# Optimization experiments

Hardware: AMD Instinct MI355X
Metric: run time of the kernel (lower is better)

The kernel has to match this reference:

```python
import jax, jax.numpy as jnp
import numpy as np

EMBED_DIM = 512
NUM_HEADS = 8
K_NEAREST = 5
B = 8192
N_MEM = 50000


def setup_inputs() -> dict:
    key = jax.random.key(0)
    ks = jax.random.split(key, 12)
    E = EMBED_DIM
    s = 1.0 / np.sqrt(E)
    inp = {
        "Q": jax.random.normal(ks[0], (B, E), jnp.float32),
        "mem_keys": jax.random.normal(ks[1], (N_MEM, E), jnp.float32),
        "mem_vals": jax.random.normal(ks[2], (N_MEM, E), jnp.float32),
        # pre-projection linears (linear_q/k/v)
        "Wq": jax.random.uniform(ks[3], (E, E), jnp.float32, -s, s),
        "bq": jnp.zeros((E,), jnp.float32),
        "Wk": jax.random.uniform(ks[4], (E, E), jnp.float32, -s, s),
        "bk": jnp.zeros((E,), jnp.float32),
        "Wv": jax.random.uniform(ks[5], (E, E), jnp.float32, -s, s),
        "bv": jnp.zeros((E,), jnp.float32),
        # nn.MultiheadAttention internal in/out projections
        "W_in_q": jax.random.uniform(ks[6], (E, E), jnp.float32, -s, s),
        "W_in_k": jax.random.uniform(ks[7], (E, E), jnp.float32, -s, s),
        "W_in_v": jax.random.uniform(ks[8], (E, E), jnp.float32, -s, s),
        "b_in": jnp.zeros((3 * E,), jnp.float32),
        "W_out": jax.random.uniform(ks[9], (E, E), jnp.float32, -s, s),
        "b_out": jnp.zeros((E,), jnp.float32),
    }
    return inp


def _find_k_nearest(Q, mem_keys, mem_vals, k):
    # squared Euclidean distance; argmax of negative distance == k nearest
    # dists: [B, N]
    sq = jnp.sum(mem_keys * mem_keys, axis=-1)  # [N]
    scores = 2.0 * (Q @ mem_keys.T) - sq[None, :]  # -||q-m||^2 up to const
    _, idx = jax.lax.top_k(scores, k)  # [B, k]
    K = mem_keys[idx]  # [B, k, E]
    V = mem_vals[idx]  # [B, k, E]
    return K, V


def _mha(Q, K, V, W_in_q, W_in_k, W_in_v, b_in, W_out, b_out):
    # Q: [B,1,E], K/V: [B,k,E]; torch nn.MultiheadAttention, batch_first
    E = Q.shape[-1]
    H = NUM_HEADS
    d = E // H
    q = Q @ W_in_q.T + b_in[:E]
    k = K @ W_in_k.T + b_in[E:2 * E]
    v = V @ W_in_v.T + b_in[2 * E:]
    Bsz = Q.shape[0]
    q = q.reshape(Bsz, -1, H, d).transpose(0, 2, 1, 3)  # [B,H,1,d]
    k = k.reshape(Bsz, -1, H, d).transpose(0, 2, 1, 3)  # [B,H,k,d]
    v = v.reshape(Bsz, -1, H, d).transpose(0, 2, 1, 3)
    scores = jnp.einsum("bhqd,bhkd->bhqk", q, k) / jnp.sqrt(jnp.float32(d))
    attn = jax.nn.softmax(scores, axis=-1)
    out = jnp.einsum("bhqk,bhkd->bhqd", attn, v)
    out = out.transpose(0, 2, 1, 3).reshape(Bsz, -1, E)
    return out @ W_out.T + b_out


def reference(Q, mem_keys, mem_vals, Wq, bq, Wk, bk, Wv, bv,
              W_in_q, W_in_k, W_in_v, b_in, W_out, b_out):
    K, V = _find_k_nearest(Q, mem_keys, mem_vals, K_NEAREST)
    Qs = Q[:, None, :]  # [B,1,E]
    Qp = Qs @ Wq.T + bq
    Kp = K @ Wk.T + bk
    Vp = V @ Wv.T + bv
    return _mha(Qp, Kp, Vp, W_in_q, W_in_k, W_in_v, b_in, W_out, b_out)
```

## Files before the change

### kernel.cpp

```cpp
#include <hip/hip_runtime.h>
#include <hip/hip_bf16.h>
#include <hip/hip_fp16.h>

typedef _Float16 f16;
typedef _Float16 f16x8 __attribute__((ext_vector_type(8)));
typedef float f32x4 __attribute__((ext_vector_type(4)));

constexpr int EE     = 512;
constexpr int NMEM   = 50000;
constexpr int BQ     = 8192;
constexpr int NSEG   = 16;
constexpr int SEGLEN = NMEM / NSEG;
constexpr int KVT    = 32;
constexpr int NT32   = (SEGLEN + KVT - 1) / KVT;
constexpr int NC     = 5;
constexpr int NCAND  = NSEG * NC;
constexpr int NRES   = 10;

typedef const __attribute__((address_space(1))) unsigned char* gas_t;
typedef __attribute__((address_space(3))) unsigned char* las_t;
__device__ static inline void g2l16(const void* g, void* l) {
  __builtin_amdgcn_global_load_lds((gas_t)g, (las_t)l, 16, 0, 0);
}

__device__ static inline float pack_si(float s, int li) {
  return __uint_as_float((__float_as_uint(s) & 0xFFFFF000u) | (unsigned)li);
}

__global__ __launch_bounds__(256) void k_prep_keys(const float* __restrict__ mk,
                                                   f16* __restrict__ kh,
                                                   float* __restrict__ sq32,
                                                   double* __restrict__ sq64) {
  int row  = blockIdx.x * 4 + (threadIdx.x >> 6);
  int lane = threadIdx.x & 63;
  const float4* src = (const float4*)(mk + (size_t)row * EE) + lane * 2;
  float4 a = src[0], b = src[1];
  double s = (double)a.x*a.x + (double)a.y*a.y + (double)a.z*a.z + (double)a.w*a.w
           + (double)b.x*b.x + (double)b.y*b.y + (double)b.z*b.z + (double)b.w*b.w;
  f16x8 h;
  h[0]=(f16)a.x; h[1]=(f16)a.y; h[2]=(f16)a.z; h[3]=(f16)a.w;
  h[4]=(f16)b.x; h[5]=(f16)b.y; h[6]=(f16)b.z; h[7]=(f16)b.w;
  *((f16x8*)(kh + (size_t)row * EE) + lane) = h;
  #pragma unroll
  for (int o = 32; o > 0; o >>= 1) s += __shfl_down(s, o);
  if (lane == 0) { sq64[row] = s; sq32[row] = (float)s; }
}

__global__ __launch_bounds__(256) void k_prep_f16(const float* __restrict__ src,
                                                  f16* __restrict__ dst) {
  int row  = blockIdx.x * 4 + (threadIdx.x >> 6);
  int lane = threadIdx.x & 63;
  const float4* s = (const float4*)(src + (size_t)row * EE) + lane * 2;
  float4 a = s[0], b = s[1];
  f16x8 h;
  h[0]=(f16)a.x; h[1]=(f16)a.y; h[2]=(f16)a.z; h[3]=(f16)a.w;
  h[4]=(f16)b.x; h[5]=(f16)b.y; h[6]=(f16)b.z; h[7]=(f16)b.w;
  *((f16x8*)(dst + (size_t)row * EE) + lane) = h;
}

__global__ __launch_bounds__(256) void k_compose(const float* __restrict__ Wq, const float* __restrict__ Wk,
                                                 const float* __restrict__ Wv, const float* __restrict__ Wiq,
                                                 const float* __restrict__ Wik, const float* __restrict__ Wiv,
                                                 f16* __restrict__ Wc) {
  int m = blockIdx.z;
  const float* A = (m == 0) ? Wiq : ((m == 1) ? Wik : Wiv);
  const float* B = (m == 0) ? Wq  : ((m == 1) ? Wk  : Wv);
  f16* C = Wc + (size_t)m * EE * EE;
  __shared__ float As[64][33];
  __shared__ float Bs[32][65];
  int i0 = blockIdx.x * 64, j0 = blockIdx.y * 64;
  int tx = threadIdx.x & 15, ty = threadIdx.x >> 4;
  float acc[4][4] = {};
  for (int kb = 0; kb < EE; kb += 32) {
    __syncthreads();
    #pragma unroll
    for (int v = 0; v < 8; ++v) {
      int idx = threadIdx.x + v * 256;
      As[idx >> 5][idx & 31] = A[(size_t)(i0 + (idx >> 5)) * EE + kb + (idx & 31)];
    }
    #pragma unroll
    for (int v = 0; v < 8; ++v) {
      int idx = threadIdx.x + v * 256;
      Bs[idx >> 6][idx & 63] = B[(size_t)(kb + (idx >> 6)) * EE + j0 + (idx & 63)];
    }
    __syncthreads();
    for (int t = 0; t < 32; ++t) {
      float av[4], bv[4];
      #pragma unroll
      for (int u = 0; u < 4; ++u) av[u] = As[ty*4+u][t];
      #pragma unroll
      for (int u = 0; u < 4; ++u) bv[u] = Bs[t][tx*4+u];
      #pragma unroll
      for (int a = 0; a < 4; ++a)
        #pragma unroll
        for (int b = 0; b < 4; ++b) acc[a][b] = fmaf(av[a], bv[b], acc[a][b]);
    }
  }
  #pragma unroll
  for (int a = 0; a < 4; ++a)
    #pragma unroll
    for (int b = 0; b < 4; ++b)
      C[(size_t)(i0 + ty*4 + a) * EE + j0 + tx*4 + b] = (f16)acc[a][b];
}

__global__ void k_bias(const float* __restrict__ Wiq, const float* __restrict__ Wik,
                       const float* __restrict__ Wiv, const float* __restrict__ bqv,
                       const float* __restrict__ bkv, const float* __restrict__ bvv,
                       const float* __restrict__ b_in, float* __restrict__ bc) {
  int m = blockIdx.x;
  const float* Wi = (m == 0) ? Wiq : ((m == 1) ? Wik : Wiv);
  const float* bb = (m == 0) ? bqv : ((m == 1) ? bkv : bvv);
  for (int i = threadIdx.x; i < EE; i += blockDim.x) {
    float s = 0.f;
    for (int t = 0; t < EE; ++t) s = fmaf(Wi[(size_t)i * EE + t], bb[t], s);
    bc[m * EE + i] = s + b_in[m * EE + i];
  }
}

__global__ void k_cvtw(const float* __restrict__ W, f16* __restrict__ Wo) {
  int i = blockIdx.x * 256 + threadIdx.x;
  Wo[i] = (f16)W[i];
}

__global__ __launch_bounds__(256, 2) void k_stage1(const f16* __restrict__ Qh,
                                                   const f16* __restrict__ Kh,
                                                   const float* __restrict__ sq32,
                                                   int* __restrict__ part_i,
                                                   float* __restrict__ part_s) {
  const int rb  = blockIdx.x;
  const int seg = blockIdx.y;
  const int tid = threadIdx.x;
  const int w   = tid >> 6;
  const int l   = tid & 63;
  const int lc  = l & 15, lp = l >> 4;
  const int seg_start = seg * SEGLEN;
  const int seg_end   = seg_start + SEGLEN;

  __shared__ f16   Bt[2][KVT * 520];
  __shared__ float sqs[2][KVT];

  const int rowbase = rb * 128 + w * 32;
  f16x8 a0[16], a1[16];
  {
    const f16* base0 = Qh + (size_t)(rowbase + lc) * EE + lp * 8;
    const f16* base1 = base0 + (size_t)16 * EE;
    #pragma unroll
    for (int ks = 0; ks < 16; ++ks) {
      asm volatile("global_load_dwordx4 %0, %1, off"
                   : "=v"(a0[ks]) : "v"(base0 + ks * 32) : "memory");
      asm volatile("global_load_dwordx4 %0, %1, off"
                   : "=v"(a1[ks]) : "v"(base1 + ks * 32) : "memory");
    }
    asm volatile("s_waitcnt vmcnt(0)" ::: "memory");
    __builtin_amdgcn_sched_barrier(0);
  }

  float ts0[NC], ts1[NC];
  #pragma unroll
  for (int i = 0; i < NC; ++i) { ts0[i] = -3.0e38f; ts1[i] = -3.0e38f; }

#define INS1(TS, PV) do { \
    if (__ballot((PV) > TS[NC-1])) { \
      float _nv = ((PV) > TS[NC-1]) ? (PV) : TS[NC-1]; \
      TS[NC-1] = _nv; \
      _Pragma("unroll") \
      for (int _i = NC - 1; _i > 0; --_i) { \
        float _mx = fmaxf(TS[_i], TS[_i-1]); \
        float _mn = fminf(TS[_i], TS[_i-1]); \
        TS[_i-1] = _mx; TS[_i] = _mn; \
      } \
    } \
  } while (0)

  #define STAGE(buf, tt) do { \
      int kk = seg_start + (tt) * KVT; \
      _Pragma("unroll") \
      for (int j = 0; j < 8; ++j) { \
        int key = kk + w * 8 + j; \
        key = key < NMEM ? key : NMEM - 1; \
        g2l16(Kh + (size_t)key * EE + l * 8, &Bt[buf][(w*8 + j) * 520]); \
      } \
      if (tid < KVT) { \
        int kq = kk + tid; \
        float v = 6.0e38f; \
        if (kq < seg_end) v = sq32[kq]; \
        sqs[buf][tid] = v; \
      } \
    } while (0)

  STAGE(0, 0);
  for (int t = 0; t < NT32; ++t) {
    const int c = t & 1;
    __syncthreads();
    if (t + 1 < NT32) STAGE(c ^ 1, t + 1);

    f32x4 A00 = {0,0,0,0}, A01 = {0,0,0,0}, A10 = {0,0,0,0}, A11 = {0,0,0,0};
    #pragma unroll
    for (int ks = 0; ks < 16; ++ks) {
      f16x8 kf0 = *(const f16x8*)&Bt[c][lc * 520 + ks * 32 + lp * 8];
      f16x8 kf1 = *(const f16x8*)&Bt[c][(16 + lc) * 520 + ks * 32 + lp * 8];
      A00 = __builtin_amdgcn_mfma_f32_16x16x32_f16(kf0, a0[ks], A00, 0, 0, 0);
      A01 = __builtin_amdgcn_mfma_f32_16x16x32_f16(kf0, a1[ks], A01, 0, 0, 0);
      A10 = __builtin_amdgcn_mfma_f32_16x16x32_f16(kf1, a0[ks], A10, 0, 0, 0);
      A11 = __builtin_amdgcn_mfma_f32_16x16x32_f16(kf1, a1[ks], A11, 0, 0, 0);
    }
    f32x4 q0 = *(const f32x4*)&sqs[c][lp * 4];
    f32x4 q1 = *(const f32x4*)&sqs[c][16 + lp * 4];
    f32x4 s00 = 2.0f * A00 - q0;
    f32x4 s01 = 2.0f * A01 - q0;
    f32x4 s10 = 2.0f * A10 - q1;
    f32x4 s11 = 2.0f * A11 - q1;
    const int li0 = t * KVT + lp * 4;
    const int li1 = li0 + 16;
    #pragma unroll
    for (int r = 0; r < 4; ++r) {
      INS1(ts0, pack_si(s00[r], li0 + r));
      INS1(ts0, pack_si(s10[r], li1 + r));
      INS1(ts1, pack_si(s01[r], li0 + r));
      INS1(ts1, pack_si(s11[r], li1 + r));
    }
  }
  #undef STAGE

  #pragma unroll
  for (int d = 16; d <= 32; d <<= 1) {
    float os[NC];
    #pragma unroll
    for (int i = 0; i < NC; ++i) os[i] = __shfl_xor(ts0[i], d);
    #pragma unroll
    for (int j = 0; j < NC; ++j) INS1(ts0, os[j]);
    #pragma unroll
    for (int i = 0; i < NC; ++i) os[i] = __shfl_xor(ts1[i], d);
    #pragma unroll
    for (int j = 0; j < NC; ++j) INS1(ts1, os[j]);
  }
#undef INS1
  if (l < 16) {
    int row = rowbase + lc;
    #pragma unroll
    for (int i = 0; i < NC; ++i) {
      unsigned u = __float_as_uint(ts0[i]);
      part_i[(size_t)row * NCAND + seg * NC + i] = seg_start + (int)(u & 0xFFFu);
      part_s[(size_t)row * NCAND + seg * NC + i] = ts0[i];
    }
  } else if (l < 32) {
    int row = rowbase + 16 + lc;
    #pragma unroll
    for (int i = 0; i < NC; ++i) {
      unsigned u = __float_as_uint(ts1[i]);
      part_i[(size_t)row * NCAND + seg * NC + i] = seg_start + (int)(u & 0xFFFu);
      part_s[(size_t)row * NCAND + seg * NC + i] = ts1[i];
    }
  }
}

__global__ __launch_bounds__(64) void k_rescore(const float* __restrict__ Q,
                                                const float* __restrict__ mk,
                                                const double* __restrict__ sq64,
                                                const int* __restrict__ part_i,
                                                const float* __restrict__ part_s,
                                                int* __restrict__ idx5) {
  const int row = blockIdx.x;
  const int l = threadIdx.x;
  const float* Qr = Q + (size_t)row * EE;
  float q[8];
  #pragma unroll
  for (int i = 0; i < 8; ++i) q[i] = Qr[l + 64*i];
  float s0 = part_s[(size_t)row * NCAND + l];
  int   i0 = part_i[(size_t)row * NCAND + l];
  float s1 = (l < NCAND - 64) ? part_s[(size_t)row * NCAND + 64 + l] : -3.0e38f;
  int   i1 = (l < NCAND - 64) ? part_i[(size_t)row * NCAND + 64 + l] : 0;

  double bs[5] = {-1e300, -1e300, -1e300, -1e300, -1e300};
  int    bi[5] = {0, 0, 0, 0, 0};
  #pragma unroll
  for (int p = 0; p < NRES; ++p) {
    bool pick0 = (s0 >= s1);
    float m  = pick0 ? s0 : s1;
    int   mi = pick0 ? i0 : i1;
    int   code = (l << 1) | (pick0 ? 0 : 1);
    #pragma unroll
    for (int o = 32; o > 0; o >>= 1) {
      float mo = __shfl_xor(m, o);
      int   io = __shfl_xor(mi, o);
      int   co = __shfl_xor(code, o);
      if (mo > m || (mo == m && co < code)) { m = mo; mi = io; code = co; }
    }
    if ((code >> 1) == l) { if (code & 1) s1 = -3.0e38f; else s0 = -3.0e38f; }
    const float* kr = mk + (size_t)mi * EE;
    double pd = 0.0;
    #pragma unroll
    for (int i = 0; i < 8; ++i) pd += (double)q[i] * (double)kr[l + 64*i];
    #pragma unroll
    for (int o = 32; o > 0; o >>= 1) pd += __shfl_down(pd, o);
    if (l == 0) {
      double s = 2.0 * pd - sq64[mi];
      if (s > bs[4]) {
        bs[4] = s; bi[4] = mi;
        #pragma unroll
        for (int i = 4; i > 0; --i) {
          if (bs[i] > bs[i-1]) {
            double tf = bs[i]; bs[i] = bs[i-1]; bs[i-1] = tf;
            int    tx = bi[i]; bi[i] = bi[i-1]; bi[i-1] = tx;
          }
        }
      }
    }
  }
  if (l == 0) {
    #pragma unroll
    for (int i = 0; i < 5; ++i) idx5[(size_t)row*5 + i] = bi[i];
  }
}

template <int GATHER, int AF16, int OUTF32>
__global__ __launch_bounds__(256) void k_pgemm128(const int* __restrict__ gidx, const void* __restrict__ Asrc,
                                                  const f16* __restrict__ B, const float* __restrict__ bias,
                                                  void* __restrict__ outp) {
  __shared__ f16 As[128][72];
  __shared__ f16 Bs[64][72];
  const int tid = threadIdx.x;
  const int wv = tid >> 6, l = tid & 63, lc = l & 15, lp = l >> 4;
  const int m0 = blockIdx.x * 128, n0 = blockIdx.y * 64;
  const int r0 = tid >> 3;
  const int cb = (tid & 7) * 8;
  const f16*   arf[4];
  const float* ar32[4];
  #pragma unroll
  for (int v = 0; v < 4; ++v) {
    int row = m0 + r0 + v * 32;
    int gi = GATHER ? gidx[row] : row;
    if (AF16) arf[v]  = (const f16*)Asrc + (size_t)gi * EE;
    else      ar32[v] = (const float*)Asrc + (size_t)gi * EE;
  }
  const f16* br0 = B + (size_t)(n0 + r0) * EE;
  const f16* br1 = B + (size_t)(n0 + r0 + 32) * EE;
  f32x4 acc[2][4] = {{{0,0,0,0},{0,0,0,0},{0,0,0,0},{0,0,0,0}},
                     {{0,0,0,0},{0,0,0,0},{0,0,0,0},{0,0,0,0}}};
  for (int kb = 0; kb < EE; kb += 64) {
    __syncthreads();
    #pragma unroll
    for (int v = 0; v < 4; ++v) {
      if (AF16) {
        *(f16x8*)&As[r0 + v*32][cb] = *(const f16x8*)(arf[v] + kb + cb);
      } else {
        float4 x0 = *(const float4*)(ar32[v] + kb + cb);
        float4 x1 = *(const float4*)(ar32[v] + kb + cb + 4);
        f16x8 h;
        h[0]=(f16)x0.x; h[1]=(f16)x0.y; h[2]=(f16)x0.z; h[3]=(f16)x0.w;
        h[4]=(f16)x1.x; h[5]=(f16)x1.y; h[6]=(f16)x1.z; h[7]=(f16)x1.w;
        *(f16x8*)&As[r0 + v*32][cb] = h;
      }
    }
    *(f16x8*)&Bs[r0][cb]      = *(const f16x8*)(br0 + kb + cb);
    *(f16x8*)&Bs[r0 + 32][cb] = *(const f16x8*)(br1 + kb + cb);
    __syncthreads();
    #pragma unroll
    for (int ks = 0; ks < 2; ++ks) {
      f16x8 a0 = *(const f16x8*)&As[wv*32 + lc][ks*32 + lp*8];
      f16x8 a1 = *(const f16x8*)&As[wv*32 + 16 + lc][ks*32 + lp*8];
      #pragma unroll
      for (int f = 0; f < 4; ++f) {
        f16x8 b = *(const f16x8*)&Bs[f*16 + lc][ks*32 + lp*8];
        acc[0][f] = __builtin_amdgcn_mfma_f32_16x16x32_f16(a0, b, acc[0][f], 0, 0, 0);
        acc[1][f] = __builtin_amdgcn_mfma_f32_16x16x32_f16(a1, b, acc[1][f], 0, 0, 0);
      }
    }
  }
  #pragma unroll
  for (int g = 0; g < 2; ++g) {
    #pragma unroll
    for (int f = 0; f < 4; ++f) {
      int col = n0 + f*16 + lc;
      float bsv = bias[col];
      #pragma unroll
      for (int rr = 0; rr < 4; ++rr) {
        int row = m0 + wv*32 + g*16 + lp*4 + rr;
        float v = acc[g][f][rr] + bsv;
        if (OUTF32) ((float*)outp)[(size_t)row * EE + col] = v;
        else        ((f16*)outp)[(size_t)row * EE + col] = (f16)v;
      }
    }
  }
}

__global__ __launch_bounds__(256) void k_attn(const f16* __restrict__ qp, const f16* __restrict__ kp,
                                              const f16* __restrict__ vp, f16* __restrict__ ao) {
  int row = blockIdx.x * 4 + (threadIdx.x >> 6);
  int l = threadIdx.x & 63;
  int h = l >> 3, sl = l & 7;
  const f16* q = qp + (size_t)row * EE + h * 64 + sl * 8;
  float qv[8];
  #pragma unroll
  for (int i = 0; i < 8; ++i) qv[i] = (float)q[i];
  float sc[5];
  #pragma unroll
  for (int j = 0; j < 5; ++j) {
    const f16* kr = kp + ((size_t)row * 5 + j) * EE + h * 64 + sl * 8;
    float p = 0.f;
    #pragma unroll
    for (int i = 0; i < 8; ++i) p = fmaf(qv[i], (float)kr[i], p);
    p += __shfl_xor(p, 1); p += __shfl_xor(p, 2); p += __shfl_xor(p, 4);
    sc[j] = p * 0.125f;
  }
  float mx = fmaxf(fmaxf(fmaxf(sc[0], sc[1]), fmaxf(sc[2], sc[3])), sc[4]);
  float sum = 0.f;
  #pragma unroll
  for (int j = 0; j < 5; ++j) { sc[j] = __expf(sc[j] - mx); sum += sc[j]; }
  float inv = 1.0f / sum;
  float o[8] = {};
  #pragma unroll
  for (int j = 0; j < 5; ++j) {
    const f16* vr = vp + ((size_t)row * 5 + j) * EE + h * 64 + sl * 8;
    float aw = sc[j] * inv;
    #pragma unroll
    for (int i = 0; i < 8; ++i) o[i] = fmaf(aw, (float)vr[i], o[i]);
  }
  f16* dst = ao + (size_t)row * EE + h * 64 + sl * 8;
  #pragma unroll
  for (int i = 0; i < 8; ++i) dst[i] = (f16)o[i];
}

extern "C" void kernel_launch(void* const* d_in, const int* in_sizes, int n_in,
                              void* d_out, int out_size, void* d_ws, size_t ws_size,
                              hipStream_t stream) {
  const float* Q    = (const float*)d_in[0];
  const float* mk   = (const float*)d_in[1];
  const float* mv   = (const float*)d_in[2];
  const float* Wq   = (const float*)d_in[3];
  const float* bq   = (const float*)d_in[4];
  const float* Wk   = (const float*)d_in[5];
  const float* bk   = (const float*)d_in[6];
  const float* Wv   = (const float*)d_in[7];
  const float* bv   = (const float*)d_in[8];
  const float* Wiq  = (const float*)d_in[9];
  const float* Wik  = (const float*)d_in[10];
  const float* Wiv  = (const float*)d_in[11];
  const float* b_in = (const float*)d_in[12];
  const float* Wo   = (const float*)d_in[13];
  const float* bo   = (const float*)d_in[14];

  char* w = (char*)d_ws;
  size_t off = 0;
  auto alloc = [&](size_t bytes) { size_t o = off; off += (bytes + 255) & ~(size_t)255; return (void*)(w + o); };
  f16*    Kh     = (f16*)   alloc((size_t)NMEM * EE * 2);
  f16*    Qh     = (f16*)   alloc((size_t)BQ * EE * 2);
  float*  sq32   = (float*) alloc((size_t)NMEM * 4);
  double* sq64   = (double*)alloc((size_t)NMEM * 8);
  f16*    Wc     = (f16*)   alloc((size_t)3 * EE * EE * 2);
  f16*    Wo16   = (f16*)   alloc((size_t)EE * EE * 2);
  float*  bc     = (float*) alloc((size_t)3 * EE * 4);
  int*    part_i = (int*)   alloc((size_t)BQ * NCAND * 4);
  float*  part_s = (float*) alloc((size_t)BQ * NCAND * 4);
  int*    idx5   = (int*)   alloc((size_t)BQ * 5 * 4);
  f16*    qp     = (f16*)   alloc((size_t)BQ * EE * 2);
  f16*    vp     = (f16*)   alloc((size_t)BQ * 5 * EE * 2);
  f16*    ao     = Qh;
  size_t need_big = off + (size_t)NMEM * EE * 2 + (size_t)BQ * 5 * EE * 2 + 4096;
  bool big = (ws_size >= need_big);
  f16* Vh = nullptr;
  f16* kp;
  if (big) {
    Vh = (f16*)alloc((size_t)NMEM * EE * 2);
    kp = (f16*)alloc((size_t)BQ * 5 * EE * 2);
  } else {
    kp = Kh;
  }
  (void)in_sizes; (void)n_in; (void)out_size;

  k_prep_keys<<<NMEM / 4, 256, 0, stream>>>(mk, Kh, sq32, sq64);
  k_prep_f16<<<BQ / 4, 256, 0, stream>>>(Q, Qh);
  if (big) k_prep_f16<<<NMEM / 4, 256, 0, stream>>>(mv, Vh);
  k_compose<<<dim3(8, 8, 3), 256, 0, stream>>>(Wq, Wk, Wv, Wiq, Wik, Wiv, Wc);
  k_bias<<<3, 256, 0, stream>>>(Wiq, Wik, Wiv, bq, bk, bv, b_in, bc);
  k_cvtw<<<(EE * EE) / 256, 256, 0, stream>>>(Wo, Wo16);
  k_stage1<<<dim3(BQ / 128, NSEG), 256, 0, stream>>>(Qh, Kh, sq32, part_i, part_s);
  k_rescore<<<BQ, 64, 0, stream>>>(Q, mk, sq64, part_i, part_s, idx5);
  k_pgemm128<0,1,0><<<dim3(BQ / 128, 8), 256, 0, stream>>>(nullptr, Qh, Wc, bc, qp);
  if (big) {
    k_pgemm128<1,1,0><<<dim3(BQ * 5 / 128, 8), 256, 0, stream>>>(idx5, Kh, Wc + (size_t)EE * EE, bc + EE, kp);
    k_pgemm128<1,1,0><<<dim3(BQ * 5 / 128, 8), 256, 0, stream>>>(idx5, Vh, Wc + (size_t)2 * EE * EE, bc + 2 * EE, vp);
  } else {
    k_pgemm128<1,0,0><<<dim3(BQ * 5 / 128, 8), 256, 0, stream>>>(idx5, mk, Wc + (size_t)EE * EE, bc + EE, kp);
    k_pgemm128<1,0,0><<<dim3(BQ * 5 / 128, 8), 256, 0, stream>>>(idx5, mv, Wc + (size_t)2 * EE * EE, bc + 2 * EE, vp);
  }
  k_attn<<<BQ / 4, 256, 0, stream>>>(qp, kp, vp, ao);
  k_pgemm128<0,1,1><<<dim3(BQ / 128, 8), 256, 0, stream>>>(nullptr, ao, Wo16, bo, d_out);
}
```

Baseline: 746.6 us.

## Pre-swizzle keys into MFMA fragment layout and load directly from global in stage1

Adds a prep kernel that converts memory keys to f16 in per-segment tiles already arranged in MFMA fragment order, with padded squared norms per tile. Stage1 then drops the LDS double buffer and __syncthreads, reading fragments straight from global/L2 with coalesced loads. The grid is linearized and remapped so blocks sharing a segment run together for L2 reuse. The cost is an extra prep pass and a bigger workspace, and stage1 now depends on global-load latency without explicit prefetching.

Result: slower. 1.500 ms (+100.9%).

```diff
diff --git a/kernel.cpp b/kernel.cpp
--- a/kernel.cpp
+++ b/kernel.cpp
@@ -13,15 +13,10 @@
 constexpr int SEGLEN = NMEM / NSEG;
 constexpr int KVT    = 32;
 constexpr int NT32   = (SEGLEN + KVT - 1) / KVT;
+constexpr int TILE_E = KVT * EE;
 constexpr int NC     = 5;
 constexpr int NCAND  = NSEG * NC;
 constexpr int NRES   = 10;
-
-typedef const __attribute__((address_space(1))) unsigned char* gas_t;
-typedef __attribute__((address_space(3))) unsigned char* las_t;
-__device__ static inline void g2l16(const void* g, void* l) {
-  __builtin_amdgcn_global_load_lds((gas_t)g, (las_t)l, 16, 0, 0);
-}
 
 __device__ static inline float pack_si(float s, int li) {
   return __uint_as_float((__float_as_uint(s) & 0xFFFFF000u) | (unsigned)li);
@@ -37,13 +32,48 @@
   float4 a = src[0], b = src[1];
   double s = (double)a.x*a.x + (double)a.y*a.y + (double)a.z*a.z + (double)a.w*a.w
            + (double)b.x*b.x + (double)b.y*b.y + (double)b.z*b.z + (double)b.w*b.w;
-  f16x8 h;
-  h[0]=(f16)a.x; h[1]=(f16)a.y; h[2]=(f16)a.z; h[3]=(f16)a.w;
-  h[4]=(f16)b.x; h[5]=(f16)b.y; h[6]=(f16)b.z; h[7]=(f16)b.w;
-  *((f16x8*)(kh + (size_t)row * EE) + lane) = h;
+  if (kh) {
+    f16x8 h;
+    h[0]=(f16)a.x; h[1]=(f16)a.y; h[2]=(f16)a.z; h[3]=(f16)a.w;
+    h[4]=(f16)b.x; h[5]=(f16)b.y; h[6]=(f16)b.z; h[7]=(f16)b.w;
+    *((f16x8*)(kh + (size_t)row * EE) + lane) = h;
+  }
   #pragma unroll
   for (int o = 32; o > 0; o >>= 1) s += __shfl_down(s, o);
   if (lane == 0) { sq64[row] = s; sq32[row] = (float)s; }
+}
+
+__global__ __launch_bounds__(256) void k_prep_kf(const float* __restrict__ mk,
+                                                 const float* __restrict__ sq32,
+                                                 f16* __restrict__ Khf,
+                                                 float* __restrict__ sqsP) {
+  const int t = blockIdx.x, s = blockIdx.y;
+  const int tid = threadIdx.x;
+  const int fg = tid >> 6, l6 = tid & 63, lc = l6 & 15, lp = l6 >> 4;
+  const size_t tb = (size_t)(s * NT32 + t) * TILE_E;
+  const int kk = t * KVT;
+  #pragma unroll
+  for (int j = 0; j < 8; ++j) {
+    int f = fg + j * 4;
+    int ks = f >> 1, half = f & 1;
+    int keyl = kk + half * 16 + lc;
+    f16x8 h;
+    #pragma unroll
+    for (int i = 0; i < 8; ++i) h[i] = (f16)0.f;
+    if (keyl < SEGLEN) {
+      const float* src = mk + (size_t)(s * SEGLEN + keyl) * EE + ks * 32 + lp * 8;
+      float4 x0 = *(const float4*)(src);
+      float4 x1 = *(const float4*)(src + 4);
+      h[0]=(f16)x0.x; h[1]=(f16)x0.y; h[2]=(f16)x0.z; h[3]=(f16)x0.w;
+      h[4]=(f16)x1.x; h[5]=(f16)x1.y; h[6]=(f16)x1.z; h[7]=(f16)x1.w;
+    }
+    *(f16x8*)(Khf + tb + (size_t)f * 512 + (size_t)l6 * 8) = h;
+  }
+  if (tid < KVT) {
+    int keyl = kk + tid;
+    sqsP[(size_t)(s * NT32 + t) * KVT + tid] =
+        (keyl < SEGLEN) ? sq32[s * SEGLEN + keyl] : 6.0e38f;
+  }
 }
 
 __global__ __launch_bounds__(256) void k_prep_f16(const float* __restrict__ src,
@@ -123,21 +153,17 @@
 }
 
 __global__ __launch_bounds__(256, 2) void k_stage1(const f16* __restrict__ Qh,
-                                                   const f16* __restrict__ Kh,
-                                                   const float* __restrict__ sq32,
+                                                   const f16* __restrict__ Khf,
+                                                   const float* __restrict__ sqsP,
                                                    int* __restrict__ part_i,
                                                    float* __restrict__ part_s) {
-  const int rb  = blockIdx.x;
-  const int seg = blockIdx.y;
+  const int h   = blockIdx.x;
+  const int seg = (h & 7) + 8 * (h >> 9);
+  const int rb  = (h >> 3) & 63;
   const int tid = threadIdx.x;
   const int w   = tid >> 6;
   const int l   = tid & 63;
   const int lc  = l & 15, lp = l >> 4;
-  const int seg_start = seg * SEGLEN;
-  const int seg_end   = seg_start + SEGLEN;
-
-  __shared__ f16   Bt[2][KVT * 520];
-  __shared__ float sqs[2][KVT];
 
   const int rowbase = rb * 128 + w * 32;
   f16x8 a0[16], a1[16];
@@ -172,40 +198,25 @@
     } \
   } while (0)
 
-  #define STAGE(buf, tt) do { \
-      int kk = seg_start + (tt) * KVT; \
-      _Pragma("unroll") \
-      for (int j = 0; j < 8; ++j) { \
-        int key = kk + w * 8 + j; \
-        key = key < NMEM ? key : NMEM - 1; \
-        g2l16(Kh + (size_t)key * EE + l * 8, &Bt[buf][(w*8 + j) * 520]); \
-      } \
-      if (tid < KVT) { \
-        int kq = kk + tid; \
-        float v = 6.0e38f; \
-        if (kq < seg_end) v = sq32[kq]; \
-        sqs[buf][tid] = v; \
-      } \
-    } while (0)
-
-  STAGE(0, 0);
+  const f16*   kf_base = Khf  + (size_t)seg * NT32 * TILE_E + (size_t)l * 8;
+  const float* sq_base = sqsP + (size_t)seg * NT32 * KVT;
+
   for (int t = 0; t < NT32; ++t) {
-    const int c = t & 1;
-    __syncthreads();
-    if (t + 1 < NT32) STAGE(c ^ 1, t + 1);
+    const f16*   kfb = kf_base + (size_t)t * TILE_E;
+    const float* sqb = sq_base + t * KVT;
+    f32x4 q0 = *(const f32x4*)(sqb + lp * 4);
+    f32x4 q1 = *(const f32x4*)(sqb + 16 + lp * 4);
 
     f32x4 A00 = {0,0,0,0}, A01 = {0,0,0,0}, A10 = {0,0,0,0}, A11 = {0,0,0,0};
     #pragma unroll
     for (int ks = 0; ks < 16; ++ks) {
-      f16x8 kf0 = *(const f16x8*)&Bt[c][lc * 520 + ks * 32 + lp * 8];
-      f16x8 kf1 = *(const f16x8*)&Bt[c][(16 + lc) * 520 + ks * 32 + lp * 8];
+      f16x8 kf0 = *(const f16x8*)(kfb + (2 * ks + 0) * 512);
+      f16x8 kf1 = *(const f16x8*)(kfb + (2 * ks + 1) * 512);
       A00 = __builtin_amdgcn_mfma_f32_16x16x32_f16(kf0, a0[ks], A00, 0, 0, 0);
       A01 = __builtin_amdgcn_mfma_f32_16x16x32_f16(kf0, a1[ks], A01, 0, 0, 0);
       A10 = __builtin_amdgcn_mfma_f32_16x16x32_f16(kf1, a0[ks], A10, 0, 0, 0);
       A11 = __builtin_amdgcn_mfma_f32_16x16x32_f16(kf1, a1[ks], A11, 0, 0, 0);
     }
-    f32x4 q0 = *(const f32x4*)&sqs[c][lp * 4];
-    f32x4 q1 = *(const f32x4*)&sqs[c][16 + lp * 4];
     f32x4 s00 = 2.0f * A00 - q0;
     f32x4 s01 = 2.0f * A01 - q0;
     f32x4 s10 = 2.0f * A10 - q1;
@@ -220,7 +231,6 @@
       INS1(ts1, pack_si(s11[r], li1 + r));
     }
   }
-  #undef STAGE
 
   #pragma unroll
   for (int d = 16; d <= 32; d <<= 1) {
@@ -235,6 +245,7 @@
     for (int j = 0; j < NC; ++j) INS1(ts1, os[j]);
   }
 #undef INS1
+  const int seg_start = seg * SEGLEN;
   if (l < 16) {
     int row = rowbase + lc;
     #pragma unroll
@@ -443,7 +454,6 @@
   char* w = (char*)d_ws;
   size_t off = 0;
   auto alloc = [&](size_t bytes) { size_t o = off; off += (bytes + 255) & ~(size_t)255; return (void*)(w + o); };
-  f16*    Kh     = (f16*)   alloc((size_t)NMEM * EE * 2);
   f16*    Qh     = (f16*)   alloc((size_t)BQ * EE * 2);
   float*  sq32   = (float*) alloc((size_t)NMEM * 4);
   double* sq64   = (double*)alloc((size_t)NMEM * 8);
@@ -455,26 +465,27 @@
   int*    idx5   = (int*)   alloc((size_t)BQ * 5 * 4);
   f16*    qp     = (f16*)   alloc((size_t)BQ * EE * 2);
   f16*    vp     = (f16*)   alloc((size_t)BQ * 5 * EE * 2);
+  f16*    Khf    = (f16*)   alloc((size_t)NSEG * NT32 * TILE_E * 2);
+  float*  sqsP   = (float*) alloc((size_t)NSEG * NT32 * KVT * 4);
   f16*    ao     = Qh;
-  size_t need_big = off + (size_t)NMEM * EE * 2 + (size_t)BQ * 5 * EE * 2 + 4096;
+  f16*    kp     = Khf;
+  size_t need_big = off + 2 * (size_t)NMEM * EE * 2 + 4096;
   bool big = (ws_size >= need_big);
-  f16* Vh = nullptr;
-  f16* kp;
+  f16* Kh = nullptr; f16* Vh = nullptr;
   if (big) {
+    Kh = (f16*)alloc((size_t)NMEM * EE * 2);
     Vh = (f16*)alloc((size_t)NMEM * EE * 2);
-    kp = (f16*)alloc((size_t)BQ * 5 * EE * 2);
-  } else {
-    kp = Kh;
   }
   (void)in_sizes; (void)n_in; (void)out_size;
 
   k_prep_keys<<<NMEM / 4, 256, 0, stream>>>(mk, Kh, sq32, sq64);
+  k_prep_kf<<<dim3(NT32, NSEG), 256, 0, stream>>>(mk, sq32, Khf, sqsP);
   k_prep_f16<<<BQ / 4, 256, 0, stream>>>(Q, Qh);
   if (big) k_prep_f16<<<NMEM / 4, 256, 0, stream>>>(mv, Vh);
   k_compose<<<dim3(8, 8, 3), 256, 0, stream>>>(Wq, Wk, Wv, Wiq, Wik, Wiv, Wc);
   k_bias<<<3, 256, 0, stream>>>(Wiq, Wik, Wiv, bq, bk, bv, b_in, bc);
   k_cvtw<<<(EE * EE) / 256, 256, 0, stream>>>(Wo, Wo16);
-  k_stage1<<<dim3(BQ / 128, NSEG), 256, 0, stream>>>(Qh, Kh, sq32, part_i, part_s);
+  k_stage1<<<dim3(64 * NSEG), 256, 0, stream>>>(Qh, Khf, sqsP, part_i, part_s);
   k_rescore<<<BQ, 64, 0, stream>>>(Q, mk, sq64, part_i, part_s, idx5);
   k_pgemm128<0,1,0><<<dim3(BQ / 128, 8), 256, 0, stream>>>(nullptr, Qh, Wc, bc, qp);
   if (big) {
```
